# Kernel tuning notes

Hardware: AMD Instinct MI355X
Metric: run time of the kernel (lower is better)

## Reference

```python
import jax, jax.numpy as jnp
import numpy as np

N = 2097152
N_LAYERS = 32
N_SUB = 8


def setup_inputs() -> dict:
    key = jax.random.key(0)
    k1, k2, k3, k4 = jax.random.split(key, 4)
    return {
        "x": jax.random.normal(k1, (N, 2), dtype=jnp.float32),
        "act_w": 0.05 * jax.random.normal(k2, (N_LAYERS,), dtype=jnp.float32),
        "bias_b": 0.05 * jax.random.normal(k3, (N_LAYERS, 2), dtype=jnp.float32),
        "lin_w": 0.05 * jax.random.normal(k4, (N_LAYERS, N_SUB), dtype=jnp.float32),
    }


def _forward_chain(q, p, act_w, bias_b, lin_w):
    # Apply Modules[0..end] with inverse=0.
    n_layers, n_sub = lin_w.shape
    for i in range(n_layers):
        # activation module: up adds w*tanh(p) to q, low adds w*tanh(q) to p
        if i % 2 == 0:
            q = q + act_w[i] * jnp.tanh(p)
        else:
            p = p + act_w[i] * jnp.tanh(q)
        # bias module (inserted at j == 0)
        q = q + bias_b[i, 0]
        p = p + bias_b[i, 1]
        # linear shear modules
        for j in range(n_sub):
            if j % 2 == 0:   # linear_module_up: q += w*p
                q = q + lin_w[i, j] * p
            else:            # linear_module_low: p += w*q
                p = p + lin_w[i, j] * q
    return q, p


def _inverse_chain(q, p, act_w, bias_b, lin_w):
    # Apply all modules in reverse order with inverse=1 (negated weights).
    n_layers, n_sub = lin_w.shape
    for i in reversed(range(n_layers)):
        for j in reversed(range(n_sub)):
            if j % 2 == 0:
                q = q - lin_w[i, j] * p
            else:
                p = p - lin_w[i, j] * q
        q = q - bias_b[i, 0]
        p = p - bias_b[i, 1]
        if i % 2 == 0:
            q = q - act_w[i] * jnp.tanh(p)
        else:
            p = p - act_w[i] * jnp.tanh(q)
    return q, p


def reference(x, act_w, bias_b, lin_w):
    q, p = x[..., 0], x[..., 1]
    q, p = _forward_chain(q, p, act_w, bias_b, lin_w)
    # time reversal: multiply by [1, -1]
    p = -p
    q, p = _inverse_chain(q, p, act_w, bias_b, lin_w)
    # final module-0 inverse is included in _inverse_chain; scale by [1, -1]
    return jnp.stack([q, -p], axis=-1)
```

## Files before the change

### kernel.cpp

```cpp
#include <hip/hip_runtime.h>

constexpr int NL = 32;
constexpr int PPT = 8;

#define C_SCALE 2.8853900817779268f
#define INV_C   0.34657359027997264f

__device__ __forceinline__ float fast_exp2(float x) {
#if __has_builtin(__builtin_amdgcn_exp2f)
    return __builtin_amdgcn_exp2f(x);
#else
    return __expf(0.69314718055994531f * x);
#endif
}

__global__ void build_tables(const float* __restrict__ act_w,
                             const float* __restrict__ bias_b,
                             const float* __restrict__ lin_w,
                             float* __restrict__ tab)
{
    int t = threadIdx.x;
    if (t >= NL) return;
    float m00 = 1.f, m01 = 0.f, m10 = 0.f, m11 = 1.f;
    #pragma unroll
    for (int j = 0; j < 8; ++j) {
        float w = lin_w[t * 8 + j];
        if ((j & 1) == 0) { m00 = fmaf(w, m10, m00); m01 = fmaf(w, m11, m01); }
        else              { m10 = fmaf(w, m00, m10); m11 = fmaf(w, m01, m11); }
    }
    float b0 = bias_b[2 * t], b1 = bias_b[2 * t + 1];
    float aw = act_w[t];
    const float c = C_SCALE;
    float awc = aw * c;

    float C0 = c * fmaf(m00, b0, m01 * b1);
    float C1 = c * fmaf(m10, b0, m11 * b1);
    if ((t & 1) == 0) { C0 = fmaf(awc, m00, C0); C1 = fmaf(awc, m10, C1); }
    else              { C0 = fmaf(awc, m01, C0); C1 = fmaf(awc, m11, C1); }
    float* f = &tab[t * 16];
    f[0] = m00; f[1] = m01; f[2] = m10; f[3] = m11;
    f[4] = C0;  f[5] = C1;  f[6] = -2.f * awc; f[7] = 0.f;

    float i00 = m11, i01 = -m01, i10 = -m10, i11 = m00;
    float D0 = -c * b0, D1 = -c * b1;
    if ((t & 1) == 0) D0 -= awc; else D1 -= awc;
    f[8]  = i00; f[9]  = i01; f[10] = i10; f[11] = i11;
    f[12] = D0;  f[13] = D1;  f[14] = 2.f * awc; f[15] = 0.f;
}

__global__ __launch_bounds__(256) void sympnet_main(
    const float* __restrict__ x,
    const float* __restrict__ tab,
    float* __restrict__ out)
{
    int gid = blockIdx.x * blockDim.x + threadIdx.x;
    const float4* x4 = (const float4*)x;
    float4* out4 = (float4*)out;
    long base = (long)gid * (PPT / 2);

    float Q[PPT], P[PPT];
    #pragma unroll
    for (int k = 0; k < PPT / 2; ++k) {
        float4 v = x4[base + k];
        Q[2*k]   = C_SCALE * v.x; P[2*k]   = C_SCALE * v.y;
        Q[2*k+1] = C_SCALE * v.z; P[2*k+1] = C_SCALE * v.w;
    }

    #pragma unroll 1
    for (int i = 0; i < NL; i += 2) {
        const float* f = &tab[i * 16];
        float m00=f[0], m01=f[1], m10=f[2], m11=f[3], C0=f[4], C1=f[5], T=f[6];
        const float* g = &tab[(i + 1) * 16];
        float n00=g[0], n01=g[1], n10=g[2], n11=g[3], E0=g[4], E1=g[5], U=g[6];
        #pragma unroll
        for (int k = 0; k < PPT; ++k) {
            float r  = __builtin_amdgcn_rcpf(fast_exp2(P[k]) + 1.0f);
            float Qa = fmaf(T, r, Q[k]);
            float Qn = fmaf(m00, Qa, fmaf(m01, P[k], C0));
            float Pn = fmaf(m10, Qa, fmaf(m11, P[k], C1));
            float r2 = __builtin_amdgcn_rcpf(fast_exp2(Qn) + 1.0f);
            float Pa = fmaf(U, r2, Pn);
            Q[k] = fmaf(n00, Qn, fmaf(n01, Pa, E0));
            P[k] = fmaf(n10, Qn, fmaf(n11, Pa, E1));
        }
    }

    #pragma unroll
    for (int k = 0; k < PPT; ++k) P[k] = -P[k];

    #pragma unroll 1
    for (int i = NL - 1; i > 0; i -= 2) {
        const float* g = &tab[i * 16 + 8];
        float n00=g[0], n01=g[1], n10=g[2], n11=g[3], E0=g[4], E1=g[5], U=g[6];
        const float* f = &tab[(i - 1) * 16 + 8];
        float m00=f[0], m01=f[1], m10=f[2], m11=f[3], C0=f[4], C1=f[5], T=f[6];
        #pragma unroll
        for (int k = 0; k < PPT; ++k) {
            float Qn = fmaf(n00, Q[k], fmaf(n01, P[k], E0));
            float Pn = fmaf(n10, Q[k], fmaf(n11, P[k], E1));
            float r  = __builtin_amdgcn_rcpf(fast_exp2(Qn) + 1.0f);
            Pn = fmaf(U, r, Pn);
            float Q2 = fmaf(m00, Qn, fmaf(m01, Pn, C0));
            float P2 = fmaf(m10, Qn, fmaf(m11, Pn, C1));
            float r2 = __builtin_amdgcn_rcpf(fast_exp2(P2) + 1.0f);
            Q[k] = fmaf(T, r2, Q2);
            P[k] = P2;
        }
    }

    #pragma unroll
    for (int k = 0; k < PPT / 2; ++k) {
        float4 o;
        o.x =  INV_C * Q[2*k];   o.y = -INV_C * P[2*k];
        o.z =  INV_C * Q[2*k+1]; o.w = -INV_C * P[2*k+1];
        out4[base + k] = o;
    }
}

extern "C" void kernel_launch(void* const* d_in, const int* in_sizes, int n_in,
                              void* d_out, int out_size, void* d_ws, size_t ws_size,
                              hipStream_t stream) {
    const float* x      = (const float*)d_in[0];
    const float* act_w  = (const float*)d_in[1];
    const float* bias_b = (const float*)d_in[2];
    const float* lin_w  = (const float*)d_in[3];
    float* out = (float*)d_out;
    float* tab = (float*)d_ws;

    build_tables<<<1, 64, 0, stream>>>(act_w, bias_b, lin_w, tab);

    int npts = in_sizes[0] / 2;
    int nthreads = npts / PPT;
    int blocks = (nthreads + 255) / 256;
    sympnet_main<<<blocks, 256, 0, stream>>>(x, tab, out);
}
```

Before: 101.4 us.

## Halve points per thread, coalesce loads, prefetch tables, fold time-reversal negation

Cuts points per thread from 8 to 4 and launches twice as many threads, with occupancy hinted via launch_bounds(256,8). Each thread now loads two float4s strided by the grid size, so global accesses coalesce. Table coefficients are read as float4s and software-prefetched one iteration ahead. The explicit time-reversal negation of P is folded into the last inverse-layer table entry. The trade-off is less per-thread ILP across points in exchange for more waves to hide the long exp/rcp latency chains.

```diff
diff --git a/kernel.cpp b/kernel.cpp
--- a/kernel.cpp
+++ b/kernel.cpp
@@ -1,7 +1,7 @@
 #include <hip/hip_runtime.h>
 
 constexpr int NL = 32;
-constexpr int PPT = 8;
+constexpr int PPT = 4;
 
 #define C_SCALE 2.8853900817779268f
 #define INV_C   0.34657359027997264f
@@ -44,76 +44,89 @@
     float i00 = m11, i01 = -m01, i10 = -m10, i11 = m00;
     float D0 = -c * b0, D1 = -c * b1;
     if ((t & 1) == 0) D0 -= awc; else D1 -= awc;
+    if (t == NL - 1) { i01 = -i01; i11 = -i11; }
     f[8]  = i00; f[9]  = i01; f[10] = i10; f[11] = i11;
     f[12] = D0;  f[13] = D1;  f[14] = 2.f * awc; f[15] = 0.f;
 }
 
-__global__ __launch_bounds__(256) void sympnet_main(
+__global__ __launch_bounds__(256, 8) void sympnet_main(
     const float* __restrict__ x,
     const float* __restrict__ tab,
     float* __restrict__ out)
 {
     int gid = blockIdx.x * blockDim.x + threadIdx.x;
+    int nthreads = gridDim.x * blockDim.x;
     const float4* x4 = (const float4*)x;
     float4* out4 = (float4*)out;
-    long base = (long)gid * (PPT / 2);
+    const float4* t4 = (const float4*)tab;
 
     float Q[PPT], P[PPT];
-    #pragma unroll
-    for (int k = 0; k < PPT / 2; ++k) {
-        float4 v = x4[base + k];
-        Q[2*k]   = C_SCALE * v.x; P[2*k]   = C_SCALE * v.y;
-        Q[2*k+1] = C_SCALE * v.z; P[2*k+1] = C_SCALE * v.w;
+    {
+        float4 v0 = x4[gid];
+        float4 v1 = x4[gid + nthreads];
+        Q[0] = C_SCALE * v0.x; P[0] = C_SCALE * v0.y;
+        Q[1] = C_SCALE * v0.z; P[1] = C_SCALE * v0.w;
+        Q[2] = C_SCALE * v1.x; P[2] = C_SCALE * v1.y;
+        Q[3] = C_SCALE * v1.z; P[3] = C_SCALE * v1.w;
     }
 
-    #pragma unroll 1
-    for (int i = 0; i < NL; i += 2) {
-        const float* f = &tab[i * 16];
-        float m00=f[0], m01=f[1], m10=f[2], m11=f[3], C0=f[4], C1=f[5], T=f[6];
-        const float* g = &tab[(i + 1) * 16];
-        float n00=g[0], n01=g[1], n10=g[2], n11=g[3], E0=g[4], E1=g[5], U=g[6];
-        #pragma unroll
-        for (int k = 0; k < PPT; ++k) {
-            float r  = __builtin_amdgcn_rcpf(fast_exp2(P[k]) + 1.0f);
-            float Qa = fmaf(T, r, Q[k]);
-            float Qn = fmaf(m00, Qa, fmaf(m01, P[k], C0));
-            float Pn = fmaf(m10, Qa, fmaf(m11, P[k], C1));
-            float r2 = __builtin_amdgcn_rcpf(fast_exp2(Qn) + 1.0f);
-            float Pa = fmaf(U, r2, Pn);
-            Q[k] = fmaf(n00, Qn, fmaf(n01, Pa, E0));
-            P[k] = fmaf(n10, Qn, fmaf(n11, Pa, E1));
+    {
+        float4 fa = t4[0], fb = t4[1];
+        float4 ga = t4[4], gb = t4[5];
+        #pragma unroll 1
+        for (int i = 0; i < NL; i += 2) {
+            int nx = (i + 2 < NL) ? (i + 2) : 0;
+            float4 nfa = t4[4 * nx],     nfb = t4[4 * nx + 1];
+            float4 nga = t4[4 * nx + 4], ngb = t4[4 * nx + 5];
+            #pragma unroll
+            for (int k = 0; k < PPT; ++k) {
+                float r  = __builtin_amdgcn_rcpf(fast_exp2(P[k]) + 1.0f);
+                float Qa = fmaf(fb.z, r, Q[k]);
+                float Qn = fmaf(fa.x, Qa, fmaf(fa.y, P[k], fb.x));
+                float Pn = fmaf(fa.z, Qa, fmaf(fa.w, P[k], fb.y));
+                float r2 = __builtin_amdgcn_rcpf(fast_exp2(Qn) + 1.0f);
+                float Pa = fmaf(gb.z, r2, Pn);
+                Q[k] = fmaf(ga.x, Qn, fmaf(ga.y, Pa, gb.x));
+                P[k] = fmaf(ga.z, Qn, fmaf(ga.w, Pa, gb.y));
+            }
+            fa = nfa; fb = nfb; ga = nga; gb = ngb;
         }
     }
 
-    #pragma unroll
-    for (int k = 0; k < PPT; ++k) P[k] = -P[k];
 
-    #pragma unroll 1
-    for (int i = NL - 1; i > 0; i -= 2) {
-        const float* g = &tab[i * 16 + 8];
-        float n00=g[0], n01=g[1], n10=g[2], n11=g[3], E0=g[4], E1=g[5], U=g[6];
-        const float* f = &tab[(i - 1) * 16 + 8];
-        float m00=f[0], m01=f[1], m10=f[2], m11=f[3], C0=f[4], C1=f[5], T=f[6];
-        #pragma unroll
-        for (int k = 0; k < PPT; ++k) {
-            float Qn = fmaf(n00, Q[k], fmaf(n01, P[k], E0));
-            float Pn = fmaf(n10, Q[k], fmaf(n11, P[k], E1));
-            float r  = __builtin_amdgcn_rcpf(fast_exp2(Qn) + 1.0f);
-            Pn = fmaf(U, r, Pn);
-            float Q2 = fmaf(m00, Qn, fmaf(m01, Pn, C0));
-            float P2 = fmaf(m10, Qn, fmaf(m11, Pn, C1));
-            float r2 = __builtin_amdgcn_rcpf(fast_exp2(P2) + 1.0f);
-            Q[k] = fmaf(T, r2, Q2);
-            P[k] = P2;
+    {
+        int i = NL - 1;
+        float4 ga = t4[4 * i + 2],       gb = t4[4 * i + 3];
+        float4 fa = t4[4 * (i - 1) + 2], fb = t4[4 * (i - 1) + 3];
+        #pragma unroll 1
+        for (; i > 0; i -= 2) {
+            int nx = (i > 2) ? (i - 2) : (NL - 1);
+            float4 nga = t4[4 * nx + 2],       ngb = t4[4 * nx + 3];
+            float4 nfa = t4[4 * (nx - 1) + 2], nfb = t4[4 * (nx - 1) + 3];
+            #pragma unroll
+            for (int k = 0; k < PPT; ++k) {
+                float Qn = fmaf(ga.x, Q[k], fmaf(ga.y, P[k], gb.x));
+                float Pn = fmaf(ga.z, Q[k], fmaf(ga.w, P[k], gb.y));
+                float r  = __builtin_amdgcn_rcpf(fast_exp2(Qn) + 1.0f);
+                Pn = fmaf(gb.z, r, Pn);
+                float Q2 = fmaf(fa.x, Qn, fmaf(fa.y, Pn, fb.x));
+                float P2 = fmaf(fa.z, Qn, fmaf(fa.w, Pn, fb.y));
+                float r2 = __builtin_amdgcn_rcpf(fast_exp2(P2) + 1.0f);
+                Q[k] = fmaf(fb.z, r2, Q2);
+                P[k] = P2;
+            }
+            ga = nga; gb = ngb; fa = nfa; fb = nfb;
         }
     }
 
-    #pragma unroll
-    for (int k = 0; k < PPT / 2; ++k) {
-        float4 o;
-        o.x =  INV_C * Q[2*k];   o.y = -INV_C * P[2*k];
-        o.z =  INV_C * Q[2*k+1]; o.w = -INV_C * P[2*k+1];
-        out4[base + k] = o;
+    {
+        float4 o0, o1;
+        o0.x =  INV_C * Q[0];  o0.y = -INV_C * P[0];
+        o0.z =  INV_C * Q[1];  o0.w = -INV_C * P[1];
+        o1.x =  INV_C * Q[2];  o1.y = -INV_C * P[2];
+        o1.z =  INV_C * Q[3];  o1.w = -INV_C * P[3];
+        out4[gid] = o0;
+        out4[gid + nthreads] = o1;
     }
 }
 
```

New measurement: 102.7 us. No clear change (+1.3%).
